# Optimization experiments

Measured on AMD Instinct MI355X. Metric: run time of the kernel, lower is better.

The kernel has to match this reference:

```python
import jax, jax.numpy as jnp
import numpy as np

N_NODES = 102400
N_EDGES = 1638400
DIMS = [128, 64, 32, 1]  # decoder_dim=128, decoder_l=3, last layer -> 1


def setup_inputs() -> dict:
    key = jax.random.key(0)
    ks = jax.random.split(key, 10)
    inp = {
        'b_z': jax.random.normal(ks[0], (N_NODES, DIMS[0]), jnp.float32),
        'src': jax.random.randint(ks[1], (N_EDGES,), 0, N_NODES, jnp.int64 if jax.config.jax_enable_x64 else jnp.int32),
        'dst': jax.random.randint(ks[2], (N_EDGES,), 0, N_NODES, jnp.int64 if jax.config.jax_enable_x64 else jnp.int32),
        'edge_weight': jax.random.uniform(ks[3], (N_EDGES,), jnp.float32),
        'b_size': 100,
    }
    # GraphConv weights: W [in, out], bias [out] (DGL xavier init; randn ok for ref)
    for i in range(3):
        inp[f'W{i}'] = jax.random.normal(ks[4 + i], (DIMS[i], DIMS[i + 1]), jnp.float32) * (1.0 / np.sqrt(DIMS[i]))
        inp[f'b{i}'] = jnp.zeros((DIMS[i + 1],), jnp.float32)
    return inp


def _gcn_layer(h, src, dst, ew, W, b, activate):
    n = h.shape[0]
    ones = jnp.ones((src.shape[0],), h.dtype)
    # norm='both': symmetric degree normalization with plain (unweighted) degrees
    out_deg = jnp.clip(jax.ops.segment_sum(ones, src, num_segments=n), 1.0)
    in_deg = jnp.clip(jax.ops.segment_sum(ones, dst, num_segments=n), 1.0)
    h = h * (out_deg ** -0.5)[:, None]
    h = h @ W  # in_feats > out_feats: transform before aggregation (DGL order)
    msg = h[src] * ew[:, None]           # [E, out] edge-weighted gather
    agg = jax.ops.segment_sum(msg, dst, num_segments=n)  # scatter-add
    agg = agg * (in_deg ** -0.5)[:, None] + b
    return jnp.tanh(agg) if activate else agg


def reference(b_z, src, dst, edge_weight, b_size, W0, b0, W1, b1, W2, b2):
    h = b_z
    h = _gcn_layer(h, src, dst, edge_weight, W0, b0, True)
    h = _gcn_layer(h, src, dst, edge_weight, W1, b1, True)
    h = _gcn_layer(h, src, dst, edge_weight, W2, b2, False)
    return h.reshape(b_size, -1)
```

## Files before the change

### kernel.cpp

```cpp
#include <hip/hip_runtime.h>
#include <hip/hip_fp16.h>
#include <math.h>

#define N_NODES 102400
#define N_EDGES 1638400
#define NB 100
#define PB 256
#define EPB (N_EDGES/PB)

union H4 { int2 i2; __half h[4]; };

__global__ __launch_bounds__(256) void histA_kernel(const int* __restrict__ src, const int* __restrict__ dst,
                                                    int* __restrict__ histD, int* __restrict__ histS) {
    __shared__ int hD[NB], hS[NB];
    int tid = threadIdx.x;
    if (tid < NB) { hD[tid] = 0; hS[tid] = 0; }
    __syncthreads();
    int base = blockIdx.x * EPB;
    for (int i = tid; i < EPB; i += 256) {
        atomicAdd(&hD[dst[base + i] >> 10], 1);
        atomicAdd(&hS[src[base + i] >> 10], 1);
    }
    __syncthreads();
    if (tid < NB) {
        histD[blockIdx.x * NB + tid] = hD[tid];
        histS[blockIdx.x * NB + tid] = hS[tid];
    }
}

__global__ __launch_bounds__(1024) void scanB_kernel(const int* __restrict__ histD, const int* __restrict__ histS,
                                                     int* __restrict__ offD, int* __restrict__ offS,
                                                     int* __restrict__ coarseD, int* __restrict__ coarseS) {
    __shared__ int pD[NB][8], pS[NB][8];
    __shared__ int baseD[NB + 1], baseS[NB + 1];
    int tid = threadIdx.x;
    int j = tid >> 3, s = tid & 7;
    if (j < NB) {
        int sd = 0, ss = 0;
        for (int k = s * 32; k < s * 32 + 32; ++k) {
            sd += histD[k * NB + j];
            ss += histS[k * NB + j];
        }
        pD[j][s] = sd; pS[j][s] = ss;
    }
    __syncthreads();
    if (tid == 0) {
        int r = 0;
        for (int q = 0; q < NB; ++q) {
            int t = 0;
            #pragma unroll
            for (int s2 = 0; s2 < 8; ++s2) t += pD[q][s2];
            baseD[q] = r; r += t;
        }
        baseD[NB] = r;
    }
    if (tid == 512) {
        int r = 0;
        for (int q = 0; q < NB; ++q) {
            int t = 0;
            #pragma unroll
            for (int s2 = 0; s2 < 8; ++s2) t += pS[q][s2];
            baseS[q] = r; r += t;
        }
        baseS[NB] = r;
    }
    __syncthreads();
    if (j < NB) {
        int r = baseD[j];
        for (int s2 = 0; s2 < s; ++s2) r += pD[j][s2];
        for (int k = s * 32; k < s * 32 + 32; ++k) { offD[k * NB + j] = r; r += histD[k * NB + j]; }
        int r2 = baseS[j];
        for (int s2 = 0; s2 < s; ++s2) r2 += pS[j][s2];
        for (int k = s * 32; k < s * 32 + 32; ++k) { offS[k * NB + j] = r2; r2 += histS[k * NB + j]; }
    }
    if (tid <= NB) coarseD[tid] = baseD[tid];
    if (tid >= 512 && tid <= 512 + NB) coarseS[tid - 512] = baseS[tid - 512];
}

__global__ __launch_bounds__(256) void partC_kernel(const int* __restrict__ src, const int* __restrict__ dst,
                                                    const float* __restrict__ ew,
                                                    const int* __restrict__ offD, const int* __restrict__ offS,
                                                    int2* __restrict__ partD, int* __restrict__ partS) {
    __shared__ int cD[NB], cS[NB];
    int tid = threadIdx.x;
    if (tid < NB) { cD[tid] = offD[blockIdx.x * NB + tid]; cS[tid] = offS[blockIdx.x * NB + tid]; }
    __syncthreads();
    int base = blockIdx.x * EPB;
    for (int i = tid; i < EPB; i += 256) {
        int s = src[base + i], d = dst[base + i];
        float w = ew[base + i];
        int p = atomicAdd(&cD[d >> 10], 1);
        partD[p] = make_int2(s | ((d & 1023) << 17), __float_as_int(w));
        int q = atomicAdd(&cS[s >> 10], 1);
        partS[q] = s & 1023;
    }
}

__global__ __launch_bounds__(1024) void fineS_kernel(const int* __restrict__ partS, const int* __restrict__ coarseS,
                                                     float* __restrict__ outdeg_inv) {
    __shared__ int hist[1024];
    int tid = threadIdx.x;
    hist[tid] = 0;
    __syncthreads();
    int beg = coarseS[blockIdx.x], end = coarseS[blockIdx.x + 1];
    for (int i = beg + tid; i < end; i += 1024) atomicAdd(&hist[partS[i]], 1);
    __syncthreads();
    outdeg_inv[blockIdx.x * 1024 + tid] = 1.0f / sqrtf((float)max(hist[tid], 1));
}

__global__ __launch_bounds__(1024) void fineD_kernel(const int2* __restrict__ partD, const int* __restrict__ coarseD,
                                                     const float* __restrict__ outdeg_inv,
                                                     int2* __restrict__ edge_perm, int* __restrict__ row_off,
                                                     float* __restrict__ indeg_inv) {
    __shared__ int hist[1024], cursor[1024];
    __shared__ int wsum[16];
    int tid = threadIdx.x, lane = tid & 63, wid = tid >> 6;
    hist[tid] = 0;
    __syncthreads();
    int beg = coarseD[blockIdx.x], end = coarseD[blockIdx.x + 1];
    for (int i = beg + tid; i < end; i += 1024) atomicAdd(&hist[(partD[i].x >> 17) & 1023], 1);
    __syncthreads();
    int v = hist[tid];
    int x = v;
    #pragma unroll
    for (int s = 1; s < 64; s <<= 1) { int t = __shfl_up(x, s, 64); if (lane >= s) x += t; }
    if (lane == 63) wsum[wid] = x;
    __syncthreads();
    if (wid == 0) {
        int ws = (lane < 16) ? wsum[lane] : 0;
        int y = ws;
        #pragma unroll
        for (int s = 1; s < 16; s <<= 1) { int t = __shfl_up(y, s, 64); if (lane >= s) y += t; }
        if (lane < 16) wsum[lane] = y - ws;
    }
    __syncthreads();
    int ex = wsum[wid] + x - v;
    cursor[tid] = beg + ex;
    int node = blockIdx.x * 1024 + tid;
    row_off[node] = beg + ex;
    indeg_inv[node] = 1.0f / sqrtf((float)max(v, 1));
    if (blockIdx.x == NB - 1 && tid == 0) row_off[N_NODES] = N_EDGES;
    __syncthreads();
    for (int i = beg + tid; i < end; i += 1024) {
        int2 t2 = partD[i];
        int d = (t2.x >> 17) & 1023, s = t2.x & 0x1FFFF;
        int p = atomicAdd(&cursor[d], 1);
        float w = __int_as_float(t2.y) * outdeg_inv[s];
        edge_perm[p] = make_int2(s, __float_as_int(w));
    }
}

template<int K, int C, int RN>
__global__ __launch_bounds__(256) void gemm_tile_kernel(
    const float* __restrict__ h, const float* __restrict__ W, __half* __restrict__ out) {
    constexpr int BM = 64;
    constexpr int RM = 4;
    constexpr int KC = 64;
    constexpr int TX = C / RN;
    constexpr int TY = BM / RM;
    static_assert(TX * TY == 256, "bad tile");
    static_assert(RN == 4, "fp16 epilogue assumes RN==4");

    __shared__ float Ws[K * C];
    __shared__ float Hs[KC][BM + 4];

    const int tid = threadIdx.x;
    const long brow = (long)blockIdx.x * BM;

    for (int i = tid; i < K * C; i += 256) Ws[i] = W[i];

    const int tx = tid % TX;
    const int ty = tid / TX;
    float acc[RM][RN] = {};

    const int lr = tid % 16;
    const int lk = tid / 16;

    for (int kc = 0; kc < K; kc += KC) {
        __syncthreads();
        #pragma unroll
        for (int p0 = 0; p0 < BM; p0 += 16) {
            const int r = p0 + lr;
            const float4 hv = *(const float4*)(h + (brow + r) * K + kc + lk * 4);
            Hs[lk * 4 + 0][r] = hv.x;
            Hs[lk * 4 + 1][r] = hv.y;
            Hs[lk * 4 + 2][r] = hv.z;
            Hs[lk * 4 + 3][r] = hv.w;
        }
        __syncthreads();

        #pragma unroll
        for (int k = 0; k < KC; ++k) {
            const float4 a4 = *(const float4*)&Hs[k][ty * RM];
            const float av[RM] = {a4.x, a4.y, a4.z, a4.w};
            float b[RN];
            *(float4*)b = *(const float4*)&Ws[(kc + k) * C + tx * RN];
            #pragma unroll
            for (int i = 0; i < RM; ++i)
                #pragma unroll
                for (int j = 0; j < RN; ++j)
                    acc[i][j] += av[i] * b[j];
        }
    }

    #pragma unroll
    for (int i = 0; i < RM; ++i) {
        const long row = brow + ty * RM + i;
        __half2 p01 = __floats2half2_rn(acc[i][0], acc[i][1]);
        __half2 p23 = __floats2half2_rn(acc[i][2], acc[i][3]);
        int2 packed = make_int2(*(int*)&p01, *(int*)&p23);
        *(int2*)(out + row * C + tx * RN) = packed;
    }
}

__global__ __launch_bounds__(256) void agg64_gemm_kernel(
    const __half* __restrict__ ht, const int* __restrict__ row_off,
    const int2* __restrict__ ep, const float* __restrict__ indeg_inv,
    const float* __restrict__ b0, const float* __restrict__ W1,
    __half* __restrict__ ht1, int N) {
    __shared__ float h1s[8][64];
    const int tid = threadIdx.x;
    const int lane = tid & 63;
    const int wv = tid >> 6;
    const int chunk = lane & 15;
    const int eslot = lane >> 4;
    const int hf = lane >> 5;
    const int c = lane & 31;

    float w1reg[32];
    #pragma unroll
    for (int j = 0; j < 32; ++j) w1reg[j] = W1[(hf * 32 + j) * 32 + c];
    const float bch = b0[(chunk << 2) | eslot];
    const char* htb = (const char*)ht;
    const unsigned coff = (unsigned)(chunk << 3);

    const int pair0 = (blockIdx.x * blockDim.x + tid) >> 6;
    const int npairs = N >> 1;
    const int nwaves = (gridDim.x * blockDim.x) >> 6;

    for (int pid = pair0; pid < npairs; pid += nwaves) {
        const int n0 = pid << 1;
        const int ro0 = row_off[n0], ro1 = row_off[n0 + 1], ro2 = row_off[n0 + 2];
        const int em0 = max(ro1 - 1, 0), em1 = max(ro2 - 1, 0);
        float4 a0 = {0, 0, 0, 0}, a1 = {0, 0, 0, 0};
        float4 c0 = {0, 0, 0, 0}, c1 = {0, 0, 0, 0};
        int e0 = ro0, e1 = ro1;
        while (true) {
            const int i00 = e0 + eslot, i01 = i00 + 4, i02 = i00 + 8, i03 = i00 + 12;
            const int j00 = e1 + eslot, j01 = j00 + 4, j02 = j00 + 8, j03 = j00 + 12;
            int2 p00 = ep[min(i00, em0)];
            int2 p01 = ep[min(i01, em0)];
            int2 p02 = ep[min(i02, em0)];
            int2 p03 = ep[min(i03, em0)];
            int2 p10 = ep[min(j00, em1)];
            int2 p11 = ep[min(j01, em1)];
            int2 p12 = ep[min(j02, em1)];
            int2 p13 = ep[min(j03, em1)];
            float w00 = (i00 < ro1) ? __int_as_float(p00.y) : 0.0f;
            float w01 = (i01 < ro1) ? __int_as_float(p01.y) : 0.0f;
            float w02 = (i02 < ro1) ? __int_as_float(p02.y) : 0.0f;
            float w03 = (i03 < ro1) ? __int_as_float(p03.y) : 0.0f;
            float w10 = (j00 < ro2) ? __int_as_float(p10.y) : 0.0f;
            float w11 = (j01 < ro2) ? __int_as_float(p11.y) : 0.0f;
            float w12 = (j02 < ro2) ? __int_as_float(p12.y) : 0.0f;
            float w13 = (j03 < ro2) ? __int_as_float(p13.y) : 0.0f;
            H4 r00, r01, r02, r03, r10, r11, r12, r13;
            r00.i2 = *(const int2*)(htb + (((unsigned)p00.x << 7) | coff));
            r01.i2 = *(const int2*)(htb + (((unsigned)p01.x << 7) | coff));
            r02.i2 = *(const int2*)(htb + (((unsigned)p02.x << 7) | coff));
            r03.i2 = *(const int2*)(htb + (((unsigned)p03.x << 7) | coff));
            r10.i2 = *(const int2*)(htb + (((unsigned)p10.x << 7) | coff));
            r11.i2 = *(const int2*)(htb + (((unsigned)p11.x << 7) | coff));
            r12.i2 = *(const int2*)(htb + (((unsigned)p12.x << 7) | coff));
            r13.i2 = *(const int2*)(htb + (((unsigned)p13.x << 7) | coff));
            a0.x = fmaf(__half2float(r00.h[0]), w00, a0.x);
            a0.y = fmaf(__half2float(r00.h[1]), w00, a0.y);
            a0.z = fmaf(__half2float(r00.h[2]), w00, a0.z);
            a0.w = fmaf(__half2float(r00.h[3]), w00, a0.w);
            a1.x = fmaf(__half2float(r01.h[0]), w01, a1.x);
            a1.y = fmaf(__half2float(r01.h[1]), w01, a1.y);
            a1.z = fmaf(__half2float(r01.h[2]), w01, a1.z);
            a1.w = fmaf(__half2float(r01.h[3]), w01, a1.w);
            a0.x = fmaf(__half2float(r02.h[0]), w02, a0.x);
            a0.y = fmaf(__half2float(r02.h[1]), w02, a0.y);
            a0.z = fmaf(__half2float(r02.h[2]), w02, a0.z);
            a0.w = fmaf(__half2float(r02.h[3]), w02, a0.w);
            a1.x = fmaf(__half2float(r03.h[0]), w03, a1.x);
            a1.y = fmaf(__half2float(r03.h[1]), w03, a1.y);
            a1.z = fmaf(__half2float(r03.h[2]), w03, a1.z);
            a1.w = fmaf(__half2float(r03.h[3]), w03, a1.w);
            c0.x = fmaf(__half2float(r10.h[0]), w10, c0.x);
            c0.y = fmaf(__half2float(r10.h[1]), w10, c0.y);
            c0.z = fmaf(__half2float(r10.h[2]), w10, c0.z);
            c0.w = fmaf(__half2float(r10.h[3]), w10, c0.w);
            c1.x = fmaf(__half2float(r11.h[0]), w11, c1.x);
            c1.y = fmaf(__half2float(r11.h[1]), w11, c1.y);
            c1.z = fmaf(__half2float(r11.h[2]), w11, c1.z);
            c1.w = fmaf(__half2float(r11.h[3]), w11, c1.w);
            c0.x = fmaf(__half2float(r12.h[0]), w12, c0.x);
            c0.y = fmaf(__half2float(r12.h[1]), w12, c0.y);
            c0.z = fmaf(__half2float(r12.h[2]), w12, c0.z);
            c0.w = fmaf(__half2float(r12.h[3]), w12, c0.w);
            c1.x = fmaf(__half2float(r13.h[0]), w13, c1.x);
            c1.y = fmaf(__half2float(r13.h[1]), w13, c1.y);
            c1.z = fmaf(__half2float(r13.h[2]), w13, c1.z);
            c1.w = fmaf(__half2float(r13.h[3]), w13, c1.w);
            e0 += 16; e1 += 16;
            if (e0 >= ro1 && e1 >= ro2) break;
        }
        a0.x += a1.x; a0.y += a1.y; a0.z += a1.z; a0.w += a1.w;
        c0.x += c1.x; c0.y += c1.y; c0.z += c1.z; c0.w += c1.w;
        #pragma unroll
        for (int s = 16; s <= 32; s <<= 1) {
            a0.x += __shfl_xor(a0.x, s, 64);
            a0.y += __shfl_xor(a0.y, s, 64);
            a0.z += __shfl_xor(a0.z, s, 64);
            a0.w += __shfl_xor(a0.w, s, 64);
            c0.x += __shfl_xor(c0.x, s, 64);
            c0.y += __shfl_xor(c0.y, s, 64);
            c0.z += __shfl_xor(c0.z, s, 64);
            c0.w += __shfl_xor(c0.w, s, 64);
        }
        const float sc0 = indeg_inv[n0], sc1 = indeg_inv[n0 + 1];
        float v0 = (eslot == 0) ? a0.x : (eslot == 1) ? a0.y : (eslot == 2) ? a0.z : a0.w;
        float v1 = (eslot == 0) ? c0.x : (eslot == 1) ? c0.y : (eslot == 2) ? c0.z : c0.w;
        v0 = tanhf(fmaf(v0, sc0, bch));
        v1 = tanhf(fmaf(v1, sc1, bch));
        const int sl = wv << 1;
        h1s[sl][(chunk << 2) | eslot] = v0;
        h1s[sl + 1][(chunk << 2) | eslot] = v1;
        asm volatile("s_waitcnt lgkmcnt(0)" ::: "memory");
        float t0 = 0.0f, t1 = 0.0f;
        #pragma unroll
        for (int j4 = 0; j4 < 8; ++j4) {
            const float4 h0 = *(const float4*)&h1s[sl][hf * 32 + j4 * 4];
            const float4 h1 = *(const float4*)&h1s[sl + 1][hf * 32 + j4 * 4];
            t0 = fmaf(h0.x, w1reg[j4 * 4 + 0], t0);
            t0 = fmaf(h0.y, w1reg[j4 * 4 + 1], t0);
            t0 = fmaf(h0.z, w1reg[j4 * 4 + 2], t0);
            t0 = fmaf(h0.w, w1reg[j4 * 4 + 3], t0);
            t1 = fmaf(h1.x, w1reg[j4 * 4 + 0], t1);
            t1 = fmaf(h1.y, w1reg[j4 * 4 + 1], t1);
            t1 = fmaf(h1.z, w1reg[j4 * 4 + 2], t1);
            t1 = fmaf(h1.w, w1reg[j4 * 4 + 3], t1);
        }
        t0 += __shfl_xor(t0, 32, 64);
        t1 += __shfl_xor(t1, 32, 64);
        if (hf == 0) {
            ht1[(long)n0 * 32 + c] = __float2half_rn(t0);
            ht1[(long)(n0 + 1) * 32 + c] = __float2half_rn(t1);
        }
    }
}

__global__ void agg32_dot_kernel(const __half* __restrict__ ht, const int* __restrict__ row_off,
                                 const int2* __restrict__ ep,
                                 const float* __restrict__ indeg_inv, const float* __restrict__ bias,
                                 const float* __restrict__ W2, float* __restrict__ ht2, int N) {
    int pid = (blockIdx.x * blockDim.x + threadIdx.x) >> 6;
    int lane = threadIdx.x & 63;
    int n0 = pid << 1;
    if (n0 >= N) return;
    int chunk = lane & 7;
    int eslot = lane >> 3;
    int ro0 = row_off[n0], ro1 = row_off[n0 + 1], ro2 = row_off[n0 + 2];
    int em0 = max(ro1 - 1, 0), em1 = max(ro2 - 1, 0);
    const char* htb = (const char*)ht;
    unsigned coff = (unsigned)(chunk << 3);
    float4 a0 = {0, 0, 0, 0}, a1 = {0, 0, 0, 0};
    float4 c0 = {0, 0, 0, 0}, c1 = {0, 0, 0, 0};
    int e0 = ro0, e1 = ro1;
    while (true) {
        int i00 = e0 + eslot, i01 = i00 + 8;
        int j00 = e1 + eslot, j01 = j00 + 8;
        int2 p00 = ep[min(i00, em0)];
        int2 p01 = ep[min(i01, em0)];
        int2 p10 = ep[min(j00, em1)];
        int2 p11 = ep[min(j01, em1)];
        float w00 = (i00 < ro1) ? __int_as_float(p00.y) : 0.0f;
        float w01 = (i01 < ro1) ? __int_as_float(p01.y) : 0.0f;
        float w10 = (j00 < ro2) ? __int_as_float(p10.y) : 0.0f;
        float w11 = (j01 < ro2) ? __int_as_float(p11.y) : 0.0f;
        H4 r00, r01, r10, r11;
        r00.i2 = *(const int2*)(htb + (((unsigned)p00.x << 6) | coff));
        r01.i2 = *(const int2*)(htb + (((unsigned)p01.x << 6) | coff));
        r10.i2 = *(const int2*)(htb + (((unsigned)p10.x << 6) | coff));
        r11.i2 = *(const int2*)(htb + (((unsigned)p11.x << 6) | coff));
        a0.x = fmaf(__half2float(r00.h[0]), w00, a0.x);
        a0.y = fmaf(__half2float(r00.h[1]), w00, a0.y);
        a0.z = fmaf(__half2float(r00.h[2]), w00, a0.z);
        a0.w = fmaf(__half2float(r00.h[3]), w00, a0.w);
        a1.x = fmaf(__half2float(r01.h[0]), w01, a1.x);
        a1.y = fmaf(__half2float(r01.h[1]), w01, a1.y);
        a1.z = fmaf(__half2float(r01.h[2]), w01, a1.z);
        a1.w = fmaf(__half2float(r01.h[3]), w01, a1.w);
        c0.x = fmaf(__half2float(r10.h[0]), w10, c0.x);
        c0.y = fmaf(__half2float(r10.h[1]), w10, c0.y);
        c0.z = fmaf(__half2float(r10.h[2]), w10, c0.z);
        c0.w = fmaf(__half2float(r10.h[3]), w10, c0.w);
        c1.x = fmaf(__half2float(r11.h[0]), w11, c1.x);
        c1.y = fmaf(__half2float(r11.h[1]), w11, c1.y);
        c1.z = fmaf(__half2float(r11.h[2]), w11, c1.z);
        c1.w = fmaf(__half2float(r11.h[3]), w11, c1.w);
        e0 += 16; e1 += 16;
        if (e0 >= ro1 && e1 >= ro2) break;
    }
    a0.x += a1.x; a0.y += a1.y; a0.z += a1.z; a0.w += a1.w;
    c0.x += c1.x; c0.y += c1.y; c0.z += c1.z; c0.w += c1.w;
    #pragma unroll
    for (int s = 8; s <= 32; s <<= 1) {
        a0.x += __shfl_xor(a0.x, s, 64);
        a0.y += __shfl_xor(a0.y, s, 64);
        a0.z += __shfl_xor(a0.z, s, 64);
        a0.w += __shfl_xor(a0.w, s, 64);
        c0.x += __shfl_xor(c0.x, s, 64);
        c0.y += __shfl_xor(c0.y, s, 64);
        c0.z += __shfl_xor(c0.z, s, 64);
        c0.w += __shfl_xor(c0.w, s, 64);
    }
    int q = eslot & 3;
    int ch = (chunk << 2) | q;
    float bb = bias[ch], ww = W2[ch];
    float sc0 = indeg_inv[n0], sc1 = indeg_inv[n0 + 1];
    float v0 = (q == 0) ? a0.x : (q == 1) ? a0.y : (q == 2) ? a0.z : a0.w;
    float v1 = (q == 0) ? c0.x : (q == 1) ? c0.y : (q == 2) ? c0.z : c0.w;
    float t0 = tanhf(fmaf(v0, sc0, bb)) * ww;
    float t1 = tanhf(fmaf(v1, sc1, bb)) * ww;
    #pragma unroll
    for (int s = 1; s <= 32; s <<= 1) {
        t0 += __shfl_xor(t0, s, 64);
        t1 += __shfl_xor(t1, s, 64);
    }
    if (lane == 0) {
        ht2[n0] = 0.5f * t0;
        ht2[n0 + 1] = 0.5f * t1;
    }
}

__global__ void agg1_kernel(const float* __restrict__ ht2, const int* __restrict__ row_off,
                            const int2* __restrict__ ep,
                            const float* __restrict__ indeg_inv, const float* __restrict__ bias,
                            float* __restrict__ out, int N) {
    int wave = (blockIdx.x * blockDim.x + threadIdx.x) >> 6;
    int lane = threadIdx.x & 63;
    int sub = lane >> 4;
    int slot = lane & 15;
    int node = wave * 4 + sub;
    if (node >= N) return;
    int beg = row_off[node], end = row_off[node + 1];
    float acc = 0.0f;
    for (int e = beg + slot; e < end; e += 16) {
        int2 t = ep[e];
        acc += ht2[t.x] * __int_as_float(t.y);
    }
    #pragma unroll
    for (int s = 1; s <= 8; s <<= 1) acc += __shfl_xor(acc, s, 64);
    if (slot == 0) out[node] = acc * indeg_inv[node] + bias[0];
}

extern "C" void kernel_launch(void* const* d_in, const int* in_sizes, int n_in,
                              void* d_out, int out_size, void* d_ws, size_t ws_size,
                              hipStream_t stream) {
    const float* b_z = (const float*)d_in[0];
    const int*   src = (const int*)d_in[1];
    const int*   dst = (const int*)d_in[2];
    const float* ew  = (const float*)d_in[3];
    const float* W0 = (const float*)d_in[5];
    const float* b0 = (const float*)d_in[6];
    const float* W1 = (const float*)d_in[7];
    const float* b1 = (const float*)d_in[8];
    const float* W2 = (const float*)d_in[9];
    const float* b2 = (const float*)d_in[10];
    float* out = (float*)d_out;

    const int N = N_NODES;
    const int E = N_EDGES;

    char* p = (char*)d_ws;
    int*   row_off    = (int*)p;            p += (size_t)(N + 4) * 4;
    float* outdeg_inv = (float*)p;          p += (size_t)N * 4;
    float* indeg_inv  = (float*)p;          p += (size_t)N * 4;
    int*   histD      = (int*)p;            p += (size_t)PB * NB * 4;
    int*   histS      = (int*)p;            p += (size_t)PB * NB * 4;
    int*   offD       = (int*)p;            p += (size_t)PB * NB * 4;
    int*   offS       = (int*)p;            p += (size_t)PB * NB * 4;
    int*   coarseD    = (int*)p;            p += (size_t)(NB + 4) * 4;
    int*   coarseS    = (int*)p;            p += (size_t)(NB + 4) * 4;
    int2*  edge_perm  = (int2*)p;           p += (size_t)E * 8;
    float* bufA       = (float*)p;          p += (size_t)N * 64 * 4;
    float* bufB       = (float*)p;
    int2*   partD = (int2*)bufA;
    int*    partS = (int*)bufB;
    __half* ht    = (__half*)bufA;
    __half* ht1   = (__half*)bufB;
    float*  ht2   = bufA;

    histA_kernel<<<PB, 256, 0, stream>>>(src, dst, histD, histS);
    scanB_kernel<<<1, 1024, 0, stream>>>(histD, histS, offD, offS, coarseD, coarseS);
    partC_kernel<<<PB, 256, 0, stream>>>(src, dst, ew, offD, offS, partD, partS);
    fineS_kernel<<<NB, 1024, 0, stream>>>(partS, coarseS, outdeg_inv);
    fineD_kernel<<<NB, 1024, 0, stream>>>(partD, coarseD, outdeg_inv, edge_perm, row_off, indeg_inv);

    gemm_tile_kernel<128, 64, 4><<<N / 64, 256, 0, stream>>>(b_z, W0, ht);

    agg64_gemm_kernel<<<2048, 256, 0, stream>>>(ht, row_off, edge_perm, indeg_inv, b0, W1, ht1, N);

    agg32_dot_kernel<<<N / 8, 256, 0, stream>>>(ht1, row_off, edge_perm, indeg_inv, b1, W2, ht2, N);

    agg1_kernel<<<N / 16, 256, 0, stream>>>(ht2, row_off, edge_perm, indeg_inv, b2, out, N);
}
```

Measured before the change: 346.9 us.

## Simplify scan kernel, shrink partS to 16-bit, retune agg launch grid

Replaces the 1024-thread two-level scan with a 256-thread version where each thread serially sums and scans one bucket's 256 per-block counts. Stores the source-partition local index as unsigned short instead of int, halving that scratch traffic. Doubles the grid of the 64-wide aggregation+GEMM kernel and adds launch bounds to the 32-wide aggregation kernel. The serial scan removes the sub-partitioning and its synchronisation but has longer per-thread dependency chains.

Result: faster. 330.2 us (-4.8%).

```diff
diff --git a/kernel.cpp b/kernel.cpp
--- a/kernel.cpp
+++ b/kernel.cpp
@@ -28,59 +28,27 @@
     }
 }
 
-__global__ __launch_bounds__(1024) void scanB_kernel(const int* __restrict__ histD, const int* __restrict__ histS,
-                                                     int* __restrict__ offD, int* __restrict__ offS,
-                                                     int* __restrict__ coarseD, int* __restrict__ coarseS) {
-    __shared__ int pD[NB][8], pS[NB][8];
-    __shared__ int baseD[NB + 1], baseS[NB + 1];
-    int tid = threadIdx.x;
-    int j = tid >> 3, s = tid & 7;
-    if (j < NB) {
-        int sd = 0, ss = 0;
-        for (int k = s * 32; k < s * 32 + 32; ++k) {
-            sd += histD[k * NB + j];
-            ss += histS[k * NB + j];
-        }
-        pD[j][s] = sd; pS[j][s] = ss;
-    }
-    __syncthreads();
-    if (tid == 0) {
-        int r = 0;
-        for (int q = 0; q < NB; ++q) {
-            int t = 0;
-            #pragma unroll
-            for (int s2 = 0; s2 < 8; ++s2) t += pD[q][s2];
-            baseD[q] = r; r += t;
-        }
-        baseD[NB] = r;
-    }
-    if (tid == 512) {
-        int r = 0;
-        for (int q = 0; q < NB; ++q) {
-            int t = 0;
-            #pragma unroll
-            for (int s2 = 0; s2 < 8; ++s2) t += pS[q][s2];
-            baseS[q] = r; r += t;
-        }
-        baseS[NB] = r;
-    }
-    __syncthreads();
-    if (j < NB) {
-        int r = baseD[j];
-        for (int s2 = 0; s2 < s; ++s2) r += pD[j][s2];
-        for (int k = s * 32; k < s * 32 + 32; ++k) { offD[k * NB + j] = r; r += histD[k * NB + j]; }
-        int r2 = baseS[j];
-        for (int s2 = 0; s2 < s; ++s2) r2 += pS[j][s2];
-        for (int k = s * 32; k < s * 32 + 32; ++k) { offS[k * NB + j] = r2; r2 += histS[k * NB + j]; }
-    }
-    if (tid <= NB) coarseD[tid] = baseD[tid];
-    if (tid >= 512 && tid <= 512 + NB) coarseS[tid - 512] = baseS[tid - 512];
+__global__ __launch_bounds__(256) void scanB_kernel(const int* __restrict__ histD, const int* __restrict__ histS,
+                                                    int* __restrict__ offD, int* __restrict__ offS,
+                                                    int* __restrict__ coarseD, int* __restrict__ coarseS) {
+    __shared__ int totD[NB], totS[NB], baseD[NB + 1], baseS[NB + 1];
+    int t = threadIdx.x;
+    if (t < NB) { int s = 0; for (int k = 0; k < PB; k++) s += histD[k * NB + t]; totD[t] = s; }
+    else if (t >= 128 && t < 128 + NB) { int j = t - 128; int s = 0; for (int k = 0; k < PB; k++) s += histS[k * NB + j]; totS[j] = s; }
+    __syncthreads();
+    if (t == 0)   { int r = 0; for (int j = 0; j < NB; j++) { baseD[j] = r; r += totD[j]; } baseD[NB] = r; }
+    if (t == 128) { int r = 0; for (int j = 0; j < NB; j++) { baseS[j] = r; r += totS[j]; } baseS[NB] = r; }
+    __syncthreads();
+    if (t < NB) { int r = baseD[t]; for (int k = 0; k < PB; k++) { offD[k * NB + t] = r; r += histD[k * NB + t]; } }
+    else if (t >= 128 && t < 128 + NB) { int j = t - 128; int r = baseS[j]; for (int k = 0; k < PB; k++) { offS[k * NB + j] = r; r += histS[k * NB + j]; } }
+    if (t <= NB) coarseD[t] = baseD[t];
+    if (t >= 128 && t <= 128 + NB) coarseS[t - 128] = baseS[t - 128];
 }
 
 __global__ __launch_bounds__(256) void partC_kernel(const int* __restrict__ src, const int* __restrict__ dst,
                                                     const float* __restrict__ ew,
                                                     const int* __restrict__ offD, const int* __restrict__ offS,
-                                                    int2* __restrict__ partD, int* __restrict__ partS) {
+                                                    int2* __restrict__ partD, unsigned short* __restrict__ partS) {
     __shared__ int cD[NB], cS[NB];
     int tid = threadIdx.x;
     if (tid < NB) { cD[tid] = offD[blockIdx.x * NB + tid]; cS[tid] = offS[blockIdx.x * NB + tid]; }
@@ -92,11 +60,11 @@
         int p = atomicAdd(&cD[d >> 10], 1);
         partD[p] = make_int2(s | ((d & 1023) << 17), __float_as_int(w));
         int q = atomicAdd(&cS[s >> 10], 1);
-        partS[q] = s & 1023;
-    }
-}
-
-__global__ __launch_bounds__(1024) void fineS_kernel(const int* __restrict__ partS, const int* __restrict__ coarseS,
+        partS[q] = (unsigned short)(s & 1023);
+    }
+}
+
+__global__ __launch_bounds__(1024) void fineS_kernel(const unsigned short* __restrict__ partS, const int* __restrict__ coarseS,
                                                      float* __restrict__ outdeg_inv) {
     __shared__ int hist[1024];
     int tid = threadIdx.x;
@@ -353,7 +321,7 @@
     }
 }
 
-__global__ void agg32_dot_kernel(const __half* __restrict__ ht, const int* __restrict__ row_off,
+__global__ __launch_bounds__(256) void agg32_dot_kernel(const __half* __restrict__ ht, const int* __restrict__ row_off,
                                  const int2* __restrict__ ep,
                                  const float* __restrict__ indeg_inv, const float* __restrict__ bias,
                                  const float* __restrict__ W2, float* __restrict__ ht2, int N) {
@@ -489,21 +457,21 @@
     int2*  edge_perm  = (int2*)p;           p += (size_t)E * 8;
     float* bufA       = (float*)p;          p += (size_t)N * 64 * 4;
     float* bufB       = (float*)p;
-    int2*   partD = (int2*)bufA;
-    int*    partS = (int*)bufB;
+    int2*           partD = (int2*)bufA;
+    unsigned short* partS = (unsigned short*)bufB;
     __half* ht    = (__half*)bufA;
     __half* ht1   = (__half*)bufB;
     float*  ht2   = bufA;
 
     histA_kernel<<<PB, 256, 0, stream>>>(src, dst, histD, histS);
-    scanB_kernel<<<1, 1024, 0, stream>>>(histD, histS, offD, offS, coarseD, coarseS);
+    scanB_kernel<<<1, 256, 0, stream>>>(histD, histS, offD, offS, coarseD, coarseS);
     partC_kernel<<<PB, 256, 0, stream>>>(src, dst, ew, offD, offS, partD, partS);
     fineS_kernel<<<NB, 1024, 0, stream>>>(partS, coarseS, outdeg_inv);
     fineD_kernel<<<NB, 1024, 0, stream>>>(partD, coarseD, outdeg_inv, edge_perm, row_off, indeg_inv);
 
     gemm_tile_kernel<128, 64, 4><<<N / 64, 256, 0, stream>>>(b_z, W0, ht);
 
-    agg64_gemm_kernel<<<2048, 256, 0, stream>>>(ht, row_off, edge_perm, indeg_inv, b0, W1, ht1, N);
+    agg64_gemm_kernel<<<4096, 256, 0, stream>>>(ht, row_off, edge_perm, indeg_inv, b0, W1, ht1, N);
 
     agg32_dot_kernel<<<N / 8, 256, 0, stream>>>(ht1, row_off, edge_perm, indeg_inv, b1, W2, ht2, N);
 
```
